# Kernel tuning notes

Measured on AMD Instinct MI355X. Metric: run time of the kernel, lower is better.

## Reference

```python
import jax, jax.numpy as jnp
import numpy as np

NUM_CLASSES = 10
PGD_NUMS = 10
ALPHA = 0.15
# Hardcoded in the original module: sign vector for 10 classes
SIGN_VEC = jnp.array([-1.0] * 4 + [1.0] * 6, dtype=jnp.float32)


def setup_inputs() -> dict:
    key = jax.random.key(0)
    k1, k2, k3 = jax.random.split(key, 3)
    B = 1048576
    logit = jax.random.normal(k1, (B, NUM_CLASSES), dtype=jnp.float32)
    y = jax.random.randint(k2, (B,), 0, NUM_CLASSES, dtype=jnp.int32)
    label_freq = jax.random.randint(k3, (NUM_CLASSES,), 0, PGD_NUMS, dtype=jnp.int32)
    return {"logit": logit, "y": y, "label_freq": label_freq}


def _compute_adv(logit, y):
    # softmax over classes, then per-class mean of softmax rows (one-hot^T @ p)
    p = jax.nn.softmax(logit, axis=-1)  # [B, C]
    sum_class_logit = jax.ops.segment_sum(p, y, num_segments=NUM_CLASSES)  # [C, C]
    counts = jax.ops.segment_sum(jnp.ones(y.shape[0], dtype=logit.dtype), y,
                                 num_segments=NUM_CLASSES)  # [C]
    counts = jnp.where(counts == 0, jnp.asarray(100.0, logit.dtype), counts)
    mean_class_logit = sum_class_logit / counts[:, None]  # [C, C]
    grad = mean_class_logit - jnp.eye(NUM_CLASSES, dtype=logit.dtype)
    # Faithful to torch: norm over dim=0 (columns), then reshape(-1,1) divides row i
    col_norm = jnp.linalg.norm(grad, axis=0)  # [C]
    grad = grad / col_norm[:, None]
    grad = ALPHA * grad * SIGN_VEC[:, None].astype(logit.dtype)
    return grad[y]  # index_select along dim 0 -> [B, C]


def reference(logit, y, label_freq):
    logit_copy = logit

    def step(l, _):
        l_new = l + _compute_adv(l, y)
        return l_new, l_new

    _, logit_steps = jax.lax.scan(step, logit, None, length=PGD_NUMS)  # [P, B, C]

    # Original: logit_news = sum_i logit_steps[label_freq[i]] * (y == i)
    # Since class masks are disjoint, this is a per-sample gather of step label_freq[y[n]].
    steps_per_sample = label_freq[y]  # [B]
    B = logit.shape[0]
    logit_news = logit_steps[steps_per_sample, jnp.arange(B)]  # [B, C]

    # mean cross-entropy
    log_p = jax.nn.log_softmax(logit_news, axis=-1)
    loss_adv = -jnp.mean(jnp.take_along_axis(log_p, y[:, None].astype(jnp.int32), axis=1))
    return loss_adv, logit_news, logit_copy
```

## Files before the change

kernel.cpp:

```cpp
#include <hip/hip_runtime.h>

#define PGD   10
#define ALPHA 0.15f
#define NTAB  32
#define NTHR  256
#define SPT   4
#define TSAMP (NTHR * SPT)
#define NSUB  8

#define WS_COUNTS 0
#define WS_STAB   320
#define WS_DGLOB  32320
#define WS_ZERO_N 33320

__device__ __forceinline__ int swz_tile(int bid, int nblk) {
    int q = nblk >> 3, r = nblk & 7;
    int xcd = bid & 7, idx = bid >> 3;
    return (xcd < r ? xcd * (q + 1) : r * (q + 1) + (xcd - r) * q) + idx;
}

__global__ void k_init(float* __restrict__ ws, float* __restrict__ out) {
    int i = blockIdx.x * blockDim.x + threadIdx.x;
    if (i == 0) out[0] = 0.f;
    int gs = gridDim.x * blockDim.x;
    for (int k = i; k < WS_ZERO_N; k += gs) ws[k] = 0.f;
}

__device__ __forceinline__ void table_phase(
    const float* __restrict__ Sg, const float* __restrict__ counts_tab,
    const float* __restrict__ Dprev,
    float* shT, float* shCnt, float* shCn, float* shD_out, int tid)
{
    if (tid < 10) {
        float s = 0.f;
        #pragma unroll
        for (int k = 0; k < NTAB; ++k) s += counts_tab[k * 10 + tid];
        shCnt[tid] = (s == 0.f) ? 100.f : s;
    }
    if (tid < 100) {
        float s = 0.f;
        #pragma unroll
        for (int k = 0; k < NTAB; ++k) s += Sg[k * 100 + tid];
        shT[tid] = s;
    }
    __syncthreads();
    if (tid < 100) {
        int c = tid / 10, j = tid - c * 10;
        shT[tid] = shT[tid] / shCnt[c] - ((c == j) ? 1.f : 0.f);
    }
    __syncthreads();
    if (tid < 10) {
        float s = 0.f;
        for (int cc = 0; cc < 10; ++cc) { float g = shT[cc * 10 + tid]; s += g * g; }
        shCn[tid] = sqrtf(s);
    }
    __syncthreads();
    if (tid < 100) {
        int c = tid / 10;
        float sign = (c < 4) ? -1.f : 1.f;
        float g = shT[tid] / shCn[c] * (ALPHA * sign);
        shD_out[tid] = (Dprev ? Dprev[tid] : 0.f) + g;
    }
    __syncthreads();
}

__device__ __forceinline__ void load4(const float* __restrict__ logit,
                                      const int* __restrict__ y,
                                      int s0, int B, float a[40], int yc[4]) {
    if (s0 + 4 <= B) {
        const float4* rp = reinterpret_cast<const float4*>(logit + (size_t)s0 * 10);
        float4 q[10];
        #pragma unroll
        for (int i = 0; i < 10; ++i) q[i] = rp[i];
        int4 yv = *reinterpret_cast<const int4*>(y + s0);
        #pragma unroll
        for (int i = 0; i < 10; ++i) {
            a[4 * i + 0] = q[i].x; a[4 * i + 1] = q[i].y;
            a[4 * i + 2] = q[i].z; a[4 * i + 3] = q[i].w;
        }
        yc[0] = yv.x; yc[1] = yv.y; yc[2] = yv.z; yc[3] = yv.w;
    } else {
        #pragma unroll
        for (int k = 0; k < 4; ++k) {
            int idx = s0 + k;
            if (idx < B) {
                yc[k] = y[idx];
                for (int j = 0; j < 10; ++j) a[k * 10 + j] = logit[(size_t)idx * 10 + j];
            } else {
                yc[k] = -1;
                for (int j = 0; j < 10; ++j) a[k * 10 + j] = 0.f;
            }
        }
    }
}

__global__ __launch_bounds__(NTHR) void k_step(
    const float* __restrict__ logit, const int* __restrict__ y,
    float* __restrict__ ws, int B, int t )
{
    __shared__ float sh_D[100];
    __shared__ float shT[100];
    __shared__ float shCnt[10];
    __shared__ float shCn[10];
    __shared__ float wtab[NSUB][100];
    __shared__ float ctab[NSUB][10];

    const int tid = threadIdx.x;
    const int tile = swz_tile(blockIdx.x, gridDim.x);

    float* counts_tab = ws + WS_COUNTS;
    float* S_tab      = ws + WS_STAB;
    float* D_glob     = ws + WS_DGLOB;

    const int s0 = tile * TSAMP + tid * SPT;
    float a[40];
    int   yc[4];
    load4(logit, y, s0, B, a, yc);

    for (int i = tid; i < NSUB * 100; i += NTHR) (&wtab[0][0])[i] = 0.f;
    if (t == 1) for (int i = tid; i < NSUB * 10; i += NTHR) (&ctab[0][0])[i] = 0.f;

    if (t >= 2) {
        table_phase(S_tab + (size_t)(t - 2) * (NTAB * 100), counts_tab,
                    (t >= 3) ? (D_glob + (size_t)(t - 3) * 100) : nullptr,
                    shT, shCnt, shCn, sh_D, tid);
        if (blockIdx.x == 0 && tid < 100) D_glob[(size_t)(t - 2) * 100 + tid] = sh_D[tid];
    }
    __syncthreads();

    const int sub = ((tid >> 6) << 1) | (tid & 1);
    #pragma unroll
    for (int k = 0; k < SPT; ++k) {
        int c = yc[k];
        if (c < 0) continue;
        float tv[10];
        #pragma unroll
        for (int j = 0; j < 10; ++j) tv[j] = a[k * 10 + j];
        if (t >= 2) {
            #pragma unroll
            for (int j = 0; j < 10; ++j) tv[j] += sh_D[c * 10 + j];
        }
        float m = tv[0];
        #pragma unroll
        for (int j = 1; j < 10; ++j) m = fmaxf(m, tv[j]);
        float s = 0.f;
        #pragma unroll
        for (int j = 0; j < 10; ++j) { tv[j] = __expf(tv[j] - m); s += tv[j]; }
        float r = 1.f / s;
        #pragma unroll
        for (int j = 0; j < 10; ++j) unsafeAtomicAdd(&wtab[sub][c * 10 + j], tv[j] * r);
        if (t == 1) unsafeAtomicAdd(&ctab[sub][c], 1.f);
    }
    __syncthreads();

    const int tb = blockIdx.x & (NTAB - 1);
    if (tid < 100) {
        float s = 0.f;
        #pragma unroll
        for (int w = 0; w < NSUB; ++w) s += wtab[w][tid];
        unsafeAtomicAdd(&S_tab[(size_t)(t - 1) * (NTAB * 100) + (size_t)tb * 100 + tid], s);
    }
    if (t == 1 && tid < 10) {
        float s = 0.f;
        #pragma unroll
        for (int w = 0; w < NSUB; ++w) s += ctab[w][tid];
        unsafeAtomicAdd(&counts_tab[tb * 10 + tid], s);
    }
}

__global__ __launch_bounds__(NTHR) void k_final(
    const float* __restrict__ logit, const int* __restrict__ y,
    const int* __restrict__ label_freq,
    float* __restrict__ out, float* __restrict__ ws, int B)
{
    __shared__ float tile_f[TSAMP * 10];
    __shared__ int   yt[TSAMP];
    __shared__ float Dall[PGD][100];
    __shared__ float shT[100];
    __shared__ float shCnt[10];
    __shared__ float shCn[10];
    __shared__ int   lf[10];
    __shared__ float wsum[4];

    const int tid = threadIdx.x;
    const int tile = swz_tile(blockIdx.x, gridDim.x);

    float* counts_tab = ws + WS_COUNTS;
    float* S_tab      = ws + WS_STAB;
    float* D_glob     = ws + WS_DGLOB;

    const size_t fbase = (size_t)tile * (TSAMP * 10);
    const size_t ftot  = (size_t)B * 10;
    float4 q[10];
    int4 yq;
    #pragma unroll
    for (int i = 0; i < 10; ++i) {
        size_t fi = fbase + (size_t)(tid + i * NTHR) * 4;
        if (fi + 4 <= ftot) {
            q[i] = *reinterpret_cast<const float4*>(logit + fi);
        } else {
            float e[4];
            #pragma unroll
            for (int e2 = 0; e2 < 4; ++e2) e[e2] = (fi + e2 < ftot) ? logit[fi + e2] : 0.f;
            q[i] = make_float4(e[0], e[1], e[2], e[3]);
        }
    }
    {
        int yi = tile * TSAMP + tid * 4;
        if (yi + 4 <= B) {
            yq = *reinterpret_cast<const int4*>(y + yi);
        } else {
            yq.x = (yi     < B) ? y[yi]     : 0;
            yq.y = (yi + 1 < B) ? y[yi + 1] : 0;
            yq.z = (yi + 2 < B) ? y[yi + 2] : 0;
            yq.w = (yi + 3 < B) ? y[yi + 3] : 0;
        }
    }

    table_phase(S_tab + (size_t)9 * (NTAB * 100), counts_tab, D_glob + 8 * 100,
                shT, shCnt, shCn, &Dall[9][0], tid);
    for (int i = tid; i < 900; i += NTHR) Dall[i / 100][i % 100] = D_glob[i];
    if (tid < 10) lf[tid] = label_freq[tid];

    float4* tp = reinterpret_cast<float4*>(tile_f);
    #pragma unroll
    for (int i = 0; i < 10; ++i) tp[tid + i * NTHR] = q[i];
    reinterpret_cast<int4*>(yt)[tid] = yq;
    __syncthreads();

    const int vfloat = (int)((ftot - fbase < (size_t)(TSAMP * 10)) ? (ftot - fbase)
                                                                   : (size_t)(TSAMP * 10));
    float* news_out = out + 1;
    float* copy_out = out + 1 + ftot;

    for (int m = tid; m < vfloat; m += NTHR) copy_out[fbase + m] = tile_f[m];
    __syncthreads();

    float acc = 0.f;
    #pragma unroll
    for (int k = 0; k < SPT; ++k) {
        int sl = tid + k * NTHR;
        int gi = tile * TSAMP + sl;
        if (gi >= B) break;
        int c = yt[sl];
        int sel = lf[c];
        float2* rp = reinterpret_cast<float2*>(tile_f + sl * 10);
        float nv[10];
        #pragma unroll
        for (int h = 0; h < 5; ++h) {
            float2 v = rp[h];
            nv[2 * h]     = v.x + Dall[sel][c * 10 + 2 * h];
            nv[2 * h + 1] = v.y + Dall[sel][c * 10 + 2 * h + 1];
        }
        #pragma unroll
        for (int h = 0; h < 5; ++h) rp[h] = make_float2(nv[2 * h], nv[2 * h + 1]);
        float m = nv[0];
        #pragma unroll
        for (int j = 1; j < 10; ++j) m = fmaxf(m, nv[j]);
        float s = 0.f;
        #pragma unroll
        for (int j = 0; j < 10; ++j) s += __expf(nv[j] - m);
        acc += __logf(s) + m - nv[c];
    }
    __syncthreads();

    for (int m = tid; m < vfloat; m += NTHR) news_out[fbase + m] = tile_f[m];

    #pragma unroll
    for (int off = 32; off > 0; off >>= 1) acc += __shfl_down(acc, off);
    if ((tid & 63) == 0) wsum[tid >> 6] = acc;
    __syncthreads();
    if (tid == 0)
        unsafeAtomicAdd(out, (wsum[0] + wsum[1] + wsum[2] + wsum[3]) / (float)B);
}

extern "C" void kernel_launch(void* const* d_in, const int* in_sizes, int n_in,
                              void* d_out, int out_size, void* d_ws, size_t ws_size,
                              hipStream_t stream) {
    const float* logit = (const float*)d_in[0];
    const int*   yy    = (const int*)d_in[1];
    const int*   lf    = (const int*)d_in[2];
    float* out = (float*)d_out;
    float* ws  = (float*)d_ws;
    int B = in_sizes[0] / 10;

    int blocks = (B + TSAMP - 1) / TSAMP;

    hipLaunchKernelGGL(k_init, dim3(64), dim3(256), 0, stream, ws, out);
    for (int t = 1; t <= PGD; ++t)
        hipLaunchKernelGGL(k_step, dim3(blocks), dim3(NTHR), 0, stream,
                           logit, yy, ws, B, t);
    hipLaunchKernelGGL(k_final, dim3(blocks), dim3(NTHR), 0, stream,
                       logit, yy, lf, out, ws, B);
}
```

Before: 648.3 us.

## Fuse PGD steps and final loss into one cooperative persistent kernel

Replaces the sequence of per-step kernels plus the final kernel with a single cooperative kernel. Each thread keeps its logits in registers across all PGD steps, and grid-wide syncs separate the per-step class-table reductions. This removes repeated global reads of the logits and the launch overhead, at the cost of grid barriers, high register pressure and limited occupancy. It falls back to the old multi-kernel path if co-residency is insufficient, and the tile swizzle is dropped.

```diff
diff --git a/kernel.cpp b/kernel.cpp
--- a/kernel.cpp
+++ b/kernel.cpp
@@ -1,23 +1,25 @@
 #include <hip/hip_runtime.h>
+#include <hip/hip_cooperative_groups.h>
+
+namespace cg = cooperative_groups;
 
 #define PGD   10
 #define ALPHA 0.15f
 #define NTAB  32
+#define NSUB  8
+
+#define FTH   512
+#define FSP   8
+#define FTS   (FTH * FSP)
+
 #define NTHR  256
 #define SPT   4
 #define TSAMP (NTHR * SPT)
-#define NSUB  8
 
 #define WS_COUNTS 0
 #define WS_STAB   320
 #define WS_DGLOB  32320
 #define WS_ZERO_N 33320
-
-__device__ __forceinline__ int swz_tile(int bid, int nblk) {
-    int q = nblk >> 3, r = nblk & 7;
-    int xcd = bid & 7, idx = bid >> 3;
-    return (xcd < r ? xcd * (q + 1) : r * (q + 1) + (xcd - r) * q) + idx;
-}
 
 __global__ void k_init(float* __restrict__ ws, float* __restrict__ out) {
     int i = blockIdx.x * blockDim.x + threadIdx.x;
@@ -28,7 +30,7 @@
 
 __device__ __forceinline__ void table_phase(
     const float* __restrict__ Sg, const float* __restrict__ counts_tab,
-    const float* __restrict__ Dprev,
+    const float* Dprev,
     float* shT, float* shCnt, float* shCn, float* shD_out, int tid)
 {
     if (tid < 10) {
@@ -66,7 +68,7 @@
 
 __device__ __forceinline__ void load4(const float* __restrict__ logit,
                                       const int* __restrict__ y,
-                                      int s0, int B, float a[40], int yc[4]) {
+                                      int s0, int B, float* a, int* yc) {
     if (s0 + 4 <= B) {
         const float4* rp = reinterpret_cast<const float4*>(logit + (size_t)s0 * 10);
         float4 q[10];
@@ -94,9 +96,160 @@
     }
 }
 
+__global__ __launch_bounds__(FTH, 2) void k_fused(
+    const float* __restrict__ logit, const int* __restrict__ y,
+    const int* __restrict__ label_freq,
+    float* __restrict__ out, float* __restrict__ ws, int B)
+{
+    cg::grid_group grid = cg::this_grid();
+
+    __shared__ float tile[FTH * 20];
+    __shared__ float Dall[PGD][100];
+    __shared__ float shT[100];
+    __shared__ float shCnt[10];
+    __shared__ float shCn[10];
+    __shared__ float wtab[NSUB][100];
+    __shared__ float ctab[NSUB][10];
+    __shared__ int   lf[10];
+    __shared__ float wsum[8];
+
+    const int tid = threadIdx.x;
+    float* counts_tab = ws + WS_COUNTS;
+    float* S_tab      = ws + WS_STAB;
+
+    const size_t ftot = (size_t)B * 10;
+    float* news_out = out + 1;
+    float* copy_out = out + 1 + ftot;
+
+    if (blockIdx.x == 0 && tid == 0) atomicExch(out, 0.f);
+    if (tid < 10) lf[tid] = label_freq[tid];
+
+    const int s0 = (blockIdx.x * FTH + tid) * FSP;
+    float a[80];
+    int   yc[8];
+    load4(logit, y, s0,     B, a,      yc);
+    load4(logit, y, s0 + 4, B, a + 40, yc + 4);
+
+    {
+        const size_t fbase = (size_t)blockIdx.x * (FTS * 10);
+        #pragma unroll
+        for (int i = 0; i < 20; ++i) {
+            size_t fi = fbase + (size_t)(tid + i * FTH) * 4;
+            if (fi + 4 <= ftot) {
+                float4 v = *reinterpret_cast<const float4*>(logit + fi);
+                *reinterpret_cast<float4*>(copy_out + fi) = v;
+            } else {
+                for (size_t e = fi; e < ftot; ++e) copy_out[e] = logit[e];
+            }
+        }
+    }
+
+    for (int t = 1; t <= PGD; ++t) {
+        for (int i = tid; i < NSUB * 100; i += FTH) (&wtab[0][0])[i] = 0.f;
+        if (t == 1) for (int i = tid; i < NSUB * 10; i += FTH) (&ctab[0][0])[i] = 0.f;
+        __syncthreads();
+
+        const int sub = ((tid >> 6) << 1) | (tid & 1);
+        #pragma unroll
+        for (int k = 0; k < FSP; ++k) {
+            int c = yc[k];
+            if (c < 0) continue;
+            float tv[10];
+            #pragma unroll
+            for (int j = 0; j < 10; ++j) tv[j] = a[k * 10 + j];
+            if (t >= 2) {
+                #pragma unroll
+                for (int j = 0; j < 10; ++j) tv[j] += Dall[t - 2][c * 10 + j];
+            }
+            float m = tv[0];
+            #pragma unroll
+            for (int j = 1; j < 10; ++j) m = fmaxf(m, tv[j]);
+            float s = 0.f;
+            #pragma unroll
+            for (int j = 0; j < 10; ++j) { tv[j] = __expf(tv[j] - m); s += tv[j]; }
+            float r = 1.f / s;
+            #pragma unroll
+            for (int j = 0; j < 10; ++j) unsafeAtomicAdd(&wtab[sub][c * 10 + j], tv[j] * r);
+            if (t == 1) unsafeAtomicAdd(&ctab[sub][c], 1.f);
+        }
+        __syncthreads();
+
+        const int tb = blockIdx.x & (NTAB - 1);
+        if (tid < 100) {
+            float s = 0.f;
+            #pragma unroll
+            for (int w = 0; w < NSUB; ++w) s += wtab[w][tid];
+            unsafeAtomicAdd(&S_tab[(size_t)(t - 1) * (NTAB * 100) + (size_t)tb * 100 + tid], s);
+        }
+        if (t == 1 && tid < 10) {
+            float s = 0.f;
+            #pragma unroll
+            for (int w = 0; w < NSUB; ++w) s += ctab[w][tid];
+            unsafeAtomicAdd(&counts_tab[tb * 10 + tid], s);
+        }
+        __threadfence();
+        grid.sync();
+        __threadfence();
+
+        table_phase(S_tab + (size_t)(t - 1) * (NTAB * 100), counts_tab,
+                    (t >= 2) ? &Dall[t - 2][0] : nullptr,
+                    shT, shCnt, shCn, &Dall[t - 1][0], tid);
+    }
+
+    float acc = 0.f;
+    const size_t fbase = (size_t)blockIdx.x * (FTS * 10);
+    for (int cc = 0; cc < 4; ++cc) {
+        __syncthreads();
+        if ((tid >> 7) == cc) {
+            const int lt = tid & 127;
+            #pragma unroll
+            for (int k = 0; k < FSP; ++k) {
+                int c = yc[k];
+                if (c < 0) continue;
+                int rrel = lt * FSP + k;
+                int sel = lf[c];
+                float nv[10];
+                #pragma unroll
+                for (int j = 0; j < 10; ++j) nv[j] = a[k * 10 + j] + Dall[sel][c * 10 + j];
+                #pragma unroll
+                for (int j = 0; j < 10; ++j) tile[rrel * 10 + j] = nv[j];
+                float m = nv[0];
+                #pragma unroll
+                for (int j = 1; j < 10; ++j) m = fmaxf(m, nv[j]);
+                float s = 0.f;
+                #pragma unroll
+                for (int j = 0; j < 10; ++j) s += __expf(nv[j] - m);
+                acc += __logf(s) + m - nv[c];
+            }
+        }
+        __syncthreads();
+        const float4* tp = reinterpret_cast<const float4*>(tile);
+        #pragma unroll
+        for (int i = 0; i < 5; ++i) {
+            size_t fo = fbase + (size_t)cc * (FTH * 20) + (size_t)(tid + i * FTH) * 4;
+            if (fo + 4 <= ftot) {
+                *reinterpret_cast<float4*>(news_out + fo) = tp[tid + i * FTH];
+            } else {
+                for (size_t e = fo; e < ftot; ++e) news_out[e] = tile[(e - fbase - (size_t)cc * (FTH * 20))];
+            }
+        }
+    }
+
+    #pragma unroll
+    for (int off = 32; off > 0; off >>= 1) acc += __shfl_down(acc, off);
+    if ((tid & 63) == 0) wsum[tid >> 6] = acc;
+    __syncthreads();
+    if (tid == 0) {
+        float b = 0.f;
+        #pragma unroll
+        for (int w = 0; w < 8; ++w) b += wsum[w];
+        unsafeAtomicAdd(out, b / (float)B);
+    }
+}
+
 __global__ __launch_bounds__(NTHR) void k_step(
     const float* __restrict__ logit, const int* __restrict__ y,
-    float* __restrict__ ws, int B, int t )
+    float* __restrict__ ws, int B, int t)
 {
     __shared__ float sh_D[100];
     __shared__ float shT[100];
@@ -106,13 +259,11 @@
     __shared__ float ctab[NSUB][10];
 
     const int tid = threadIdx.x;
-    const int tile = swz_tile(blockIdx.x, gridDim.x);
-
     float* counts_tab = ws + WS_COUNTS;
     float* S_tab      = ws + WS_STAB;
     float* D_glob     = ws + WS_DGLOB;
 
-    const int s0 = tile * TSAMP + tid * SPT;
+    const int s0 = (blockIdx.x * NTHR + tid) * SPT;
     float a[40];
     int   yc[4];
     load4(logit, y, s0, B, a, yc);
@@ -183,13 +334,11 @@
     __shared__ float wsum[4];
 
     const int tid = threadIdx.x;
-    const int tile = swz_tile(blockIdx.x, gridDim.x);
-
     float* counts_tab = ws + WS_COUNTS;
     float* S_tab      = ws + WS_STAB;
     float* D_glob     = ws + WS_DGLOB;
 
-    const size_t fbase = (size_t)tile * (TSAMP * 10);
+    const size_t fbase = (size_t)blockIdx.x * (TSAMP * 10);
     const size_t ftot  = (size_t)B * 10;
     float4 q[10];
     int4 yq;
@@ -206,11 +355,11 @@
         }
     }
     {
-        int yi = tile * TSAMP + tid * 4;
+        int yi = blockIdx.x * TSAMP + tid * 4;
         if (yi + 4 <= B) {
             yq = *reinterpret_cast<const int4*>(y + yi);
         } else {
-            yq.x = (yi     < B) ? y[yi]     : 0;
+            yq.x = (yi < B) ? y[yi] : 0;
             yq.y = (yi + 1 < B) ? y[yi + 1] : 0;
             yq.z = (yi + 2 < B) ? y[yi + 2] : 0;
             yq.w = (yi + 3 < B) ? y[yi + 3] : 0;
@@ -240,7 +389,7 @@
     #pragma unroll
     for (int k = 0; k < SPT; ++k) {
         int sl = tid + k * NTHR;
-        int gi = tile * TSAMP + sl;
+        int gi = blockIdx.x * TSAMP + sl;
         if (gi >= B) break;
         int c = yt[sl];
         int sel = lf[c];
@@ -284,12 +433,28 @@
     float* ws  = (float*)d_ws;
     int B = in_sizes[0] / 10;
 
-    int blocks = (B + TSAMP - 1) / TSAMP;
+    int fblocks = (B + FTS - 1) / FTS;
+
+    int dev = 0; hipGetDevice(&dev);
+    int numCU = 0;
+    hipDeviceGetAttribute(&numCU, hipDeviceAttributeMultiprocessorCount, dev);
+    int maxB = 0;
+    hipOccupancyMaxActiveBlocksPerMultiprocessor(&maxB, (const void*)k_fused, FTH, 0);
+    bool coop_ok = (maxB > 0) && ((long)maxB * (long)numCU >= (long)fblocks);
 
     hipLaunchKernelGGL(k_init, dim3(64), dim3(256), 0, stream, ws, out);
-    for (int t = 1; t <= PGD; ++t)
-        hipLaunchKernelGGL(k_step, dim3(blocks), dim3(NTHR), 0, stream,
-                           logit, yy, ws, B, t);
-    hipLaunchKernelGGL(k_final, dim3(blocks), dim3(NTHR), 0, stream,
-                       logit, yy, lf, out, ws, B);
-}
+
+    if (coop_ok) {
+        void* args[] = { (void*)&logit, (void*)&yy, (void*)&lf,
+                         (void*)&out, (void*)&ws, (void*)&B };
+        hipLaunchCooperativeKernel((const void*)k_fused, dim3(fblocks), dim3(FTH),
+                                   args, 0, stream);
+    } else {
+        int blocks = (B + TSAMP - 1) / TSAMP;
+        for (int t = 1; t <= PGD; ++t)
+            hipLaunchKernelGGL(k_step, dim3(blocks), dim3(NTHR), 0, stream,
+                               logit, yy, ws, B, t);
+        hipLaunchKernelGGL(k_final, dim3(blocks), dim3(NTHR), 0, stream,
+                           logit, yy, lf, out, ws, B);
+    }
+}
```

Measured after the change: 645.7 us. No clear change (-0.4%).
